# Kernel optimization log

Measured on AMD Instinct MI355X. Metric: run time of the kernel, lower is better.

## Reference

```python
import jax, jax.numpy as jnp
import numpy as np

N, E = 50000, 800000
IN_DIM, HID, H, L = 256, 128, 4, 2
HD = HID // H
EPS = 1e-5


def _bn(x, g, b):
    # training-mode BatchNorm1d: biased variance over batch dim, eps=1e-5
    m = x.mean(0)
    v = jnp.var(x, axis=0)
    return g * (x - m) * jax.lax.rsqrt(v + EPS) + b


def _seg_softmax(scores, dst, n):
    # scores: [E, H]; softmax over edges sharing the same dst node
    m = jax.ops.segment_max(scores, dst, num_segments=n)  # [N, H]
    e = jnp.exp(scores - m[dst])
    s = jax.ops.segment_sum(e, dst, num_segments=n)
    return e / s[dst]


def _attn_layer(h, src, dst, wq, bq, wk, bk, wv, bv, wo, bo):
    n = h.shape[0]
    scale = 1.0 / np.sqrt(HD)
    Q = (h @ wq + bq).reshape(n, H, HD)
    K = (h @ wk + bk).reshape(n, H, HD)
    V = (h @ wv + bv).reshape(n, H, HD)
    # per-edge scores: Q of src dotted with K of dst
    scores = jnp.einsum('ehd,ehd->eh', Q[src], K[dst]) * scale  # [E, H]
    attn = _seg_softmax(scores, dst, n)                         # [E, H]
    # weighted scatter-sum of V gathered at dst (faithful to source)
    out = jax.ops.segment_sum(attn[:, :, None] * V[dst], dst, num_segments=n)
    out = out.reshape(n, HID) @ wo + bo
    return jax.nn.relu(out)


def setup_inputs() -> dict:
    key = jax.random.key(0)
    ks = jax.random.split(key, 20)
    s = 0.05  # weight scale to keep activations tame
    inp = {
        'x': jax.random.normal(ks[0], (N, IN_DIM), jnp.float32),
        'edge_index': jax.random.randint(ks[1], (2, E), 0, N),
        'W_enc1': jax.random.normal(ks[2], (IN_DIM, HID), jnp.float32) * s,
        'b_enc1': jax.random.normal(ks[3], (HID,), jnp.float32) * s,
        'g1': jnp.ones((HID,), jnp.float32),
        'beta1': jnp.zeros((HID,), jnp.float32),
        'W_enc2': jax.random.normal(ks[4], (HID, HID), jnp.float32) * s,
        'b_enc2': jax.random.normal(ks[5], (HID,), jnp.float32) * s,
        'g2': jnp.ones((HID,), jnp.float32),
        'beta2': jnp.zeros((HID,), jnp.float32),
        'Wq': jax.random.normal(ks[6], (L, HID, HID), jnp.float32) * s,
        'bq': jax.random.normal(ks[7], (L, HID), jnp.float32) * s,
        'Wk': jax.random.normal(ks[8], (L, HID, HID), jnp.float32) * s,
        'bk': jax.random.normal(ks[9], (L, HID), jnp.float32) * s,
        'Wv': jax.random.normal(ks[10], (L, HID, HID), jnp.float32) * s,
        'bv': jax.random.normal(ks[11], (L, HID), jnp.float32) * s,
        'Wo': jax.random.normal(ks[12], (L, HID, HID), jnp.float32) * s,
        'bo': jax.random.normal(ks[13], (L, HID), jnp.float32) * s,
    }
    return inp


def reference(x, edge_index, W_enc1, b_enc1, g1, beta1, W_enc2, b_enc2, g2, beta2,
              Wq, bq, Wk, bk, Wv, bv, Wo, bo):
    src, dst = edge_index[0], edge_index[1]
    # encoder: Linear -> BN -> ReLU -> (dropout=id) -> Linear -> BN -> ReLU
    h = jax.nn.relu(_bn(x @ W_enc1 + b_enc1, g1, beta1))
    h = jax.nn.relu(_bn(h @ W_enc2 + b_enc2, g2, beta2))
    for i in range(L):
        h = _attn_layer(h, src, dst, Wq[i], bq[i], Wk[i], bk[i],
                        Wv[i], bv[i], Wo[i], bo[i])
    return h
```

## Files before the change

### kernel.cpp

```cpp
#include <hip/hip_runtime.h>

#define NN 50000
#define NE 800000
#define NB 1563
#define TOTF 114688

typedef unsigned short u16;
typedef unsigned int u32;
typedef __attribute__((ext_vector_type(8))) short s8v;
typedef __attribute__((ext_vector_type(4))) float f4v;

__device__ __forceinline__ void split2(float f, u16& h, u16& lo) {
    u32 u = __float_as_uint(f);
    h = (u16)(u >> 16);
    float r = f - __uint_as_float(u & 0xFFFF0000u);
    lo = (u16)(__float_as_uint(r) >> 16);
}

__global__ void scatter_prep_k(const int* __restrict__ dst, float* __restrict__ mask,
                               const float* __restrict__ W1, const float* __restrict__ W2,
                               const float* __restrict__ Wv, const float* __restrict__ Wo,
                               u16* __restrict__ fh, u16* __restrict__ fl) {
    int i = blockIdx.x * 256 + threadIdx.x;
    if (i < NE) mask[dst[i]] = 1.0f;
    if (i < TOTF) {
        const float* W;
        int local;
        if (i < 32768) { W = W1; local = i; }
        else {
            int t = i - 32768;
            int m = t >> 14;
            local = t & 16383;
            if (m == 0) W = W2;
            else if (m == 1) W = Wv;
            else if (m == 2) W = Wo;
            else if (m == 3) W = Wv + 16384;
            else W = Wo + 16384;
        }
        int j = local & 7, l = (local >> 3) & 63, nt = (local >> 9) & 7, kc = local >> 12;
        int k = kc * 32 + ((l >> 4) << 3) + j;
        int n = nt * 16 + (l & 15);
        u16 h, lo;
        split2(W[k * 128 + n], h, lo);
        fh[i] = h;
        fl[i] = lo;
    }
}

__global__ __launch_bounds__(64)
void redstats_k(const float* __restrict__ pst, float* __restrict__ st) {
    int c = blockIdx.x;
    float s = 0.f;
    for (int b = threadIdx.x; b < NB; b += 64) s += pst[(size_t)c * NB + b];
    s += __shfl_xor(s, 1);  s += __shfl_xor(s, 2);  s += __shfl_xor(s, 4);
    s += __shfl_xor(s, 8);  s += __shfl_xor(s, 16); s += __shfl_xor(s, 32);
    if (threadIdx.x == 0) st[c] = s;
}

template<int KC, int FOLD, int STATS>
__global__ __launch_bounds__(256, 8)
void mgemm_k(const float* __restrict__ A,
             const u16* __restrict__ fh, const u16* __restrict__ fl,
             const float* __restrict__ bias,
             const float* __restrict__ fst,
             const float* __restrict__ fg, const float* __restrict__ fbe,
             float* __restrict__ pst,
             float* __restrict__ C) {
    constexpr int KP = KC / 4;
    __shared__ __align__(16) u16 Ah[32][136];
    __shared__ __align__(16) u16 Al[32][136];
    __shared__ float scl[128], shf[128];
    const int tid = threadIdx.x;
    const int l = tid & 63, w = tid >> 6;
    const int q = l >> 4, cc = l & 15;
    const int sl = w >> 1, hf = w & 1;
    const int row0 = blockIdx.x * 32;

    if (FOLD && tid < 128) {
        float mean = fst[tid] * (1.0f / NN);
        float var = fst[128 + tid] * (1.0f / NN) - mean * mean;
        float rstd = rsqrtf(var + 1e-5f);
        float ga = fg[tid] * rstd;
        scl[tid] = ga;
        shf[tid] = fbe[tid] - mean * ga;
    }

    f4v zf = {0.f, 0.f, 0.f, 0.f};
    f4v acc[4];
#pragma unroll
    for (int t = 0; t < 4; ++t) acc[t] = zf;

    for (int p = 0; p < KP; ++p) {
        if (p > 0 || FOLD) __syncthreads();
#pragma unroll
        for (int it = 0; it < 4; ++it) {
            int lin = tid + 256 * it;
            int r = lin >> 5;
            int c4 = (lin & 31) * 4;
            int gr = row0 + r; if (gr > NN - 1) gr = NN - 1;
            float4 f = *(const float4*)(A + (size_t)gr * (KC * 32) + p * 128 + c4);
            float v[4] = {f.x, f.y, f.z, f.w};
            if (FOLD) {
#pragma unroll
                for (int m = 0; m < 4; ++m) {
                    float t = v[m] * scl[c4 + m] + shf[c4 + m];
                    v[m] = t > 0.f ? t : 0.f;
                }
            }
            ushort4 uh, ul;
            split2(v[0], uh.x, ul.x); split2(v[1], uh.y, ul.y);
            split2(v[2], uh.z, ul.z); split2(v[3], uh.w, ul.w);
            *(ushort4*)&Ah[r][c4] = uh;
            *(ushort4*)&Al[r][c4] = ul;
        }
        __syncthreads();
#pragma unroll
        for (int kc = 0; kc < 4; ++kc) {
            int kcg = p * 4 + kc;
            s8v ah = *(const s8v*)&Ah[16 * sl + cc][kc * 32 + q * 8];
            s8v al = *(const s8v*)&Al[16 * sl + cc][kc * 32 + q * 8];
#pragma unroll
            for (int t = 0; t < 4; ++t) {
                const int fo = kcg * 4096 + (4 * hf + t) * 512 + l * 8;
                s8v bh = *(const s8v*)(fh + fo);
                s8v bl = *(const s8v*)(fl + fo);
                acc[t] = __builtin_amdgcn_mfma_f32_16x16x32_bf16(ah, bh, acc[t], 0, 0, 0);
                acc[t] = __builtin_amdgcn_mfma_f32_16x16x32_bf16(ah, bl, acc[t], 0, 0, 0);
                acc[t] = __builtin_amdgcn_mfma_f32_16x16x32_bf16(al, bh, acc[t], 0, 0, 0);
            }
        }
    }

    float ps[4], pq[4];
#pragma unroll
    for (int t = 0; t < 4; ++t) { ps[t] = 0.f; pq[t] = 0.f; }
#pragma unroll
    for (int t = 0; t < 4; ++t) {
        int col = (4 * hf + t) * 16 + cc;
        float bb = bias[col];
#pragma unroll
        for (int r = 0; r < 4; ++r) {
            int gr = row0 + 16 * sl + q * 4 + r;
            float val = acc[t][r] + bb;
            if (gr < NN) {
                C[(size_t)gr * 128 + col] = val;
                if (STATS) { ps[t] += val; pq[t] += val * val; }
            }
        }
    }
    if (STATS) {
        __syncthreads();
        float* wredS = (float*)&Ah[0][0];
        float* wredQ = wredS + 256;
#pragma unroll
        for (int t = 0; t < 4; ++t) {
            ps[t] += __shfl_xor(ps[t], 16); ps[t] += __shfl_xor(ps[t], 32);
            pq[t] += __shfl_xor(pq[t], 16); pq[t] += __shfl_xor(pq[t], 32);
        }
        if (l < 16) {
#pragma unroll
            for (int t = 0; t < 4; ++t) {
                int col = (4 * hf + t) * 16 + l;
                wredS[sl * 128 + col] = ps[t];
                wredQ[sl * 128 + col] = pq[t];
            }
        }
        __syncthreads();
        int c = tid & 127;
        const float* src = (tid < 128) ? wredS : wredQ;
        pst[(size_t)tid * NB + blockIdx.x] = src[c] + src[128 + c];
    }
}

__global__ __launch_bounds__(256, 8)
void mmega_k(const float* __restrict__ X,
             const u16* __restrict__ fh, const u16* __restrict__ fl,
             const float* __restrict__ bv, const float* __restrict__ bo,
             const float* __restrict__ fst,
             const float* __restrict__ fg, const float* __restrict__ fbe,
             const float* __restrict__ mask, float* __restrict__ out) {
    __shared__ __align__(16) u16 Ah[32][136];
    __shared__ __align__(16) u16 Al[32][136];
    __shared__ float scl[128], shf[128];
    const int tid = threadIdx.x;
    const int l = tid & 63, w = tid >> 6;
    const int q = l >> 4, cc = l & 15;
    const int sl = w >> 1, hf = w & 1;
    const int row0 = blockIdx.x * 32;

    if (tid < 128) {
        float mean = fst[tid] * (1.0f / NN);
        float var = fst[128 + tid] * (1.0f / NN) - mean * mean;
        float rstd = rsqrtf(var + 1e-5f);
        float ga = fg[tid] * rstd;
        scl[tid] = ga;
        shf[tid] = fbe[tid] - mean * ga;
    }
    __syncthreads();

    float rm[4];
#pragma unroll
    for (int r = 0; r < 4; ++r) {
        int gr = row0 + 16 * sl + q * 4 + r;
        rm[r] = (gr < NN) ? mask[gr] : 0.f;
    }

#pragma unroll
    for (int it = 0; it < 4; ++it) {
        int lin = tid + 256 * it;
        int r = lin >> 5;
        int c4 = (lin & 31) * 4;
        int gr = row0 + r; if (gr > NN - 1) gr = NN - 1;
        float4 f = *(const float4*)(X + (size_t)gr * 128 + c4);
        float v[4] = {f.x, f.y, f.z, f.w};
        ushort4 uh, ul;
#pragma unroll
        for (int m = 0; m < 4; ++m) {
            float t = v[m] * scl[c4 + m] + shf[c4 + m];
            v[m] = t > 0.f ? t : 0.f;
        }
        split2(v[0], uh.x, ul.x); split2(v[1], uh.y, ul.y);
        split2(v[2], uh.z, ul.z); split2(v[3], uh.w, ul.w);
        *(ushort4*)&Ah[r][c4] = uh;
        *(ushort4*)&Al[r][c4] = ul;
    }
    __syncthreads();

    f4v zf = {0.f, 0.f, 0.f, 0.f};
    for (int s = 0; s < 4; ++s) {
        const u16* WH = fh + s * 16384;
        const u16* WL = fl + s * 16384;
        const float* bp = (s == 0) ? bv : (s == 1) ? bo : (s == 2) ? (bv + 128) : (bo + 128);

        f4v acc[4];
#pragma unroll
        for (int t = 0; t < 4; ++t) acc[t] = zf;
#pragma unroll
        for (int kc = 0; kc < 4; ++kc) {
            s8v ah = *(const s8v*)&Ah[16 * sl + cc][kc * 32 + q * 8];
            s8v al = *(const s8v*)&Al[16 * sl + cc][kc * 32 + q * 8];
#pragma unroll
            for (int t = 0; t < 4; ++t) {
                const int fo = kc * 4096 + (4 * hf + t) * 512 + l * 8;
                s8v bh = *(const s8v*)(WH + fo);
                s8v bl = *(const s8v*)(WL + fo);
                acc[t] = __builtin_amdgcn_mfma_f32_16x16x32_bf16(ah, bh, acc[t], 0, 0, 0);
                acc[t] = __builtin_amdgcn_mfma_f32_16x16x32_bf16(ah, bl, acc[t], 0, 0, 0);
                acc[t] = __builtin_amdgcn_mfma_f32_16x16x32_bf16(al, bh, acc[t], 0, 0, 0);
            }
        }

        if (s == 3) {
#pragma unroll
            for (int t = 0; t < 4; ++t) {
                int col = (4 * hf + t) * 16 + cc;
                float bb = bp[col];
#pragma unroll
                for (int r = 0; r < 4; ++r) {
                    int gr = row0 + 16 * sl + q * 4 + r;
                    if (gr < NN)
                        out[(size_t)gr * 128 + col] = fmaxf(acc[t][r] + bb, 0.f);
                }
            }
        } else {
            __syncthreads();
#pragma unroll
            for (int t = 0; t < 4; ++t) {
                int col = (4 * hf + t) * 16 + cc;
                float bb = bp[col];
#pragma unroll
                for (int r = 0; r < 4; ++r) {
                    int rl = 16 * sl + q * 4 + r;
                    float val = acc[t][r] + bb;
                    val = (s == 1) ? fmaxf(val, 0.f) : val * rm[r];
                    u16 h, lo; split2(val, h, lo);
                    Ah[rl][col] = h;
                    Al[rl][col] = lo;
                }
            }
            __syncthreads();
        }
    }
}

extern "C" void kernel_launch(void* const* d_in, const int* in_sizes, int n_in,
                              void* d_out, int out_size, void* d_ws, size_t ws_size,
                              hipStream_t stream) {
    const float* x   = (const float*)d_in[0];
    const int*   ei  = (const int*)d_in[1];
    const float* W1  = (const float*)d_in[2];
    const float* b1  = (const float*)d_in[3];
    const float* g1  = (const float*)d_in[4];
    const float* be1 = (const float*)d_in[5];
    const float* W2  = (const float*)d_in[6];
    const float* b2  = (const float*)d_in[7];
    const float* g2  = (const float*)d_in[8];
    const float* be2 = (const float*)d_in[9];
    const float* Wv  = (const float*)d_in[14];
    const float* bv  = (const float*)d_in[15];
    const float* Wo  = (const float*)d_in[16];
    const float* bo  = (const float*)d_in[17];

    float* out = (float*)d_out;

    char* ws = (char*)d_ws;
    float* buf  = (float*)(ws);
    float* mask = (float*)(ws + 25600000);
    float* st1  = (float*)(ws + 25800704);
    float* st2  = st1 + 256;
    u16*   fH   = (u16*)(ws + 25804800);
    u16*   fL   = fH + TOTF;
    float* pst  = (float*)(ws + 26263552);

    hipMemsetAsync(mask, 0, NN * sizeof(float), stream);
    scatter_prep_k<<<dim3((NE + 255) / 256), dim3(256), 0, stream>>>(
        ei + NE, mask, W1, W2, Wv, Wo, fH, fL);

    dim3 gg(NB), bb(256);
    mgemm_k<8, 0, 1><<<gg, bb, 0, stream>>>(x, fH, fL, b1,
                                            nullptr, nullptr, nullptr, pst, buf);
    redstats_k<<<dim3(256), dim3(64), 0, stream>>>(pst, st1);
    mgemm_k<4, 1, 1><<<gg, bb, 0, stream>>>(buf, fH + 32768, fL + 32768, b2,
                                            st1, g1, be1, pst, out);
    redstats_k<<<dim3(256), dim3(64), 0, stream>>>(pst, st2);
    mmega_k<<<gg, bb, 0, stream>>>(out, fH + 49152, fL + 49152, bv, bo,
                                   st2, g2, be2, mask, out);
}
```

Before: 226.3 us.

## Fuse BN stat reduction into GEMM tail via atomic tickets; prefetch next A chunk

```diff
diff --git a/kernel.cpp b/kernel.cpp
--- a/kernel.cpp
+++ b/kernel.cpp
@@ -4,6 +4,7 @@
 #define NE 800000
 #define NB 1563
 #define TOTF 114688
+#define TAILB 256
 
 typedef unsigned short u16;
 typedef unsigned int u32;
@@ -20,8 +21,10 @@
 __global__ void scatter_prep_k(const int* __restrict__ dst, float* __restrict__ mask,
                                const float* __restrict__ W1, const float* __restrict__ W2,
                                const float* __restrict__ Wv, const float* __restrict__ Wo,
-                               u16* __restrict__ fh, u16* __restrict__ fl) {
+                               u16* __restrict__ fh, u16* __restrict__ fl,
+                               u32* __restrict__ tickets) {
     int i = blockIdx.x * 256 + threadIdx.x;
+    if (i < 2) tickets[i] = 0;
     if (i < NE) mask[dst[i]] = 1.0f;
     if (i < TOTF) {
         const float* W;
@@ -47,16 +50,6 @@
     }
 }
 
-__global__ __launch_bounds__(64)
-void redstats_k(const float* __restrict__ pst, float* __restrict__ st) {
-    int c = blockIdx.x;
-    float s = 0.f;
-    for (int b = threadIdx.x; b < NB; b += 64) s += pst[(size_t)c * NB + b];
-    s += __shfl_xor(s, 1);  s += __shfl_xor(s, 2);  s += __shfl_xor(s, 4);
-    s += __shfl_xor(s, 8);  s += __shfl_xor(s, 16); s += __shfl_xor(s, 32);
-    if (threadIdx.x == 0) st[c] = s;
-}
-
 template<int KC, int FOLD, int STATS>
 __global__ __launch_bounds__(256, 8)
 void mgemm_k(const float* __restrict__ A,
@@ -65,11 +58,14 @@
              const float* __restrict__ fst,
              const float* __restrict__ fg, const float* __restrict__ fbe,
              float* __restrict__ pst,
+             u32* __restrict__ tick,
+             float* __restrict__ stout,
              float* __restrict__ C) {
     constexpr int KP = KC / 4;
     __shared__ __align__(16) u16 Ah[32][136];
     __shared__ __align__(16) u16 Al[32][136];
     __shared__ float scl[128], shf[128];
+    __shared__ u32 tkt;
     const int tid = threadIdx.x;
     const int l = tid & 63, w = tid >> 6;
     const int q = l >> 4, cc = l & 15;
@@ -90,6 +86,16 @@
 #pragma unroll
     for (int t = 0; t < 4; ++t) acc[t] = zf;
 
+    float4 pref[4];
+#pragma unroll
+    for (int it = 0; it < 4; ++it) {
+        int lin = tid + 256 * it;
+        int r = lin >> 5;
+        int c4 = (lin & 31) * 4;
+        int gr = row0 + r; if (gr > NN - 1) gr = NN - 1;
+        pref[it] = *(const float4*)(A + (size_t)gr * (KC * 32) + c4);
+    }
+
     for (int p = 0; p < KP; ++p) {
         if (p > 0 || FOLD) __syncthreads();
 #pragma unroll
@@ -97,9 +103,7 @@
             int lin = tid + 256 * it;
             int r = lin >> 5;
             int c4 = (lin & 31) * 4;
-            int gr = row0 + r; if (gr > NN - 1) gr = NN - 1;
-            float4 f = *(const float4*)(A + (size_t)gr * (KC * 32) + p * 128 + c4);
-            float v[4] = {f.x, f.y, f.z, f.w};
+            float v[4] = {pref[it].x, pref[it].y, pref[it].z, pref[it].w};
             if (FOLD) {
 #pragma unroll
                 for (int m = 0; m < 4; ++m) {
@@ -114,6 +118,16 @@
             *(ushort4*)&Al[r][c4] = ul;
         }
         __syncthreads();
+        if (p + 1 < KP) {
+#pragma unroll
+            for (int it = 0; it < 4; ++it) {
+                int lin = tid + 256 * it;
+                int r = lin >> 5;
+                int c4 = (lin & 31) * 4;
+                int gr = row0 + r; if (gr > NN - 1) gr = NN - 1;
+                pref[it] = *(const float4*)(A + (size_t)gr * (KC * 32) + (p + 1) * 128 + c4);
+            }
+        }
 #pragma unroll
         for (int kc = 0; kc < 4; ++kc) {
             int kcg = p * 4 + kc;
@@ -166,9 +180,37 @@
             }
         }
         __syncthreads();
-        int c = tid & 127;
-        const float* src = (tid < 128) ? wredS : wredQ;
-        pst[(size_t)tid * NB + blockIdx.x] = src[c] + src[128 + c];
+        {
+            int c = tid & 127;
+            const float* src = (tid < 128) ? wredS : wredQ;
+            __hip_atomic_store(&pst[(size_t)blockIdx.x * 256 + tid],
+                               src[c] + src[128 + c],
+                               __ATOMIC_RELAXED, __HIP_MEMORY_SCOPE_AGENT);
+        }
+        __syncthreads();
+        if (tid == 0)
+            tkt = __hip_atomic_fetch_add(tick, 1u, __ATOMIC_ACQ_REL,
+                                         __HIP_MEMORY_SCOPE_AGENT);
+        __syncthreads();
+        u32 t = tkt;
+        if (t >= (u32)(NB - TAILB) && t < (u32)NB) {
+            int c = (int)(t - (u32)(NB - TAILB));
+            if (tid == 0) {
+                while (__hip_atomic_load(tick, __ATOMIC_ACQUIRE,
+                                         __HIP_MEMORY_SCOPE_AGENT) < (u32)NB)
+                    __builtin_amdgcn_s_sleep(2);
+            }
+            __syncthreads();
+            if (tid < 64) {
+                float s = 0.f;
+                for (int b = tid; b < NB; b += 64)
+                    s += __hip_atomic_load(&pst[(size_t)b * 256 + c],
+                                           __ATOMIC_RELAXED, __HIP_MEMORY_SCOPE_AGENT);
+                s += __shfl_xor(s, 1);  s += __shfl_xor(s, 2);  s += __shfl_xor(s, 4);
+                s += __shfl_xor(s, 8);  s += __shfl_xor(s, 16); s += __shfl_xor(s, 32);
+                if (tid == 0) stout[c] = s;
+            }
+        }
     }
 }
 
@@ -308,21 +350,22 @@
     float* mask = (float*)(ws + 25600000);
     float* st1  = (float*)(ws + 25800704);
     float* st2  = st1 + 256;
+    u32*   tks  = (u32*)(ws + 25802752);
     u16*   fH   = (u16*)(ws + 25804800);
     u16*   fL   = fH + TOTF;
     float* pst  = (float*)(ws + 26263552);
 
     hipMemsetAsync(mask, 0, NN * sizeof(float), stream);
     scatter_prep_k<<<dim3((NE + 255) / 256), dim3(256), 0, stream>>>(
-        ei + NE, mask, W1, W2, Wv, Wo, fH, fL);
+        ei + NE, mask, W1, W2, Wv, Wo, fH, fL, tks);
 
     dim3 gg(NB), bb(256);
     mgemm_k<8, 0, 1><<<gg, bb, 0, stream>>>(x, fH, fL, b1,
-                                            nullptr, nullptr, nullptr, pst, buf);
-    redstats_k<<<dim3(256), dim3(64), 0, stream>>>(pst, st1);
+                                            nullptr, nullptr, nullptr,
+                                            pst, tks, st1, buf);
     mgemm_k<4, 1, 1><<<gg, bb, 0, stream>>>(buf, fH + 32768, fL + 32768, b2,
-                                            st1, g1, be1, pst, out);
-    redstats_k<<<dim3(256), dim3(64), 0, stream>>>(pst, st2);
+                                            st1, g1, be1,
+                                            pst, tks + 1, st2, out);
     mmega_k<<<gg, bb, 0, stream>>>(out, fH + 49152, fL + 49152, bv, bo,
                                    st2, g2, be2, mask, out);
 }
```

Result: slower. 409.5 us (+81.0%).

## Fold mask scatter into first GEMM, prefetch A tiles, halve mmega block

Applied to the files above, without the earlier changes.

```diff
diff --git a/kernel.cpp b/kernel.cpp
--- a/kernel.cpp
+++ b/kernel.cpp
@@ -3,6 +3,7 @@
 #define NN 50000
 #define NE 800000
 #define NB 1563
+#define NBM 3125
 #define TOTF 114688
 
 typedef unsigned short u16;
@@ -17,12 +18,12 @@
     lo = (u16)(__float_as_uint(r) >> 16);
 }
 
-__global__ void scatter_prep_k(const int* __restrict__ dst, float* __restrict__ mask,
-                               const float* __restrict__ W1, const float* __restrict__ W2,
-                               const float* __restrict__ Wv, const float* __restrict__ Wo,
-                               u16* __restrict__ fh, u16* __restrict__ fl) {
+__global__ void prep_k(float* __restrict__ mask,
+                       const float* __restrict__ W1, const float* __restrict__ W2,
+                       const float* __restrict__ Wv, const float* __restrict__ Wo,
+                       u16* __restrict__ fh, u16* __restrict__ fl) {
     int i = blockIdx.x * 256 + threadIdx.x;
-    if (i < NE) mask[dst[i]] = 1.0f;
+    if (i < NN) mask[i] = 0.f;
     if (i < TOTF) {
         const float* W;
         int local;
@@ -57,13 +58,15 @@
     if (threadIdx.x == 0) st[c] = s;
 }
 
-template<int KC, int FOLD, int STATS>
+template<int KC, int FOLD, int STATS, int SCAT>
 __global__ __launch_bounds__(256, 8)
 void mgemm_k(const float* __restrict__ A,
              const u16* __restrict__ fh, const u16* __restrict__ fl,
              const float* __restrict__ bias,
              const float* __restrict__ fst,
              const float* __restrict__ fg, const float* __restrict__ fbe,
+             const int* __restrict__ dstv,
+             float* __restrict__ maskw,
              float* __restrict__ pst,
              float* __restrict__ C) {
     constexpr int KP = KC / 4;
@@ -76,6 +79,15 @@
     const int sl = w >> 1, hf = w & 1;
     const int row0 = blockIdx.x * 32;
 
+    if (SCAT) {
+        int e2 = (blockIdx.x * 256 + tid) * 2;
+        if (e2 + 1 < NE) {
+            int2 dd = *(const int2*)(dstv + e2);
+            maskw[dd.x] = 1.0f;
+            maskw[dd.y] = 1.0f;
+        }
+    }
+
     if (FOLD && tid < 128) {
         float mean = fst[tid] * (1.0f / NN);
         float var = fst[128 + tid] * (1.0f / NN) - mean * mean;
@@ -90,6 +102,16 @@
 #pragma unroll
     for (int t = 0; t < 4; ++t) acc[t] = zf;
 
+    float4 pref[4];
+#pragma unroll
+    for (int it = 0; it < 4; ++it) {
+        int lin = tid + 256 * it;
+        int r = lin >> 5;
+        int c4 = (lin & 31) * 4;
+        int gr = row0 + r; if (gr > NN - 1) gr = NN - 1;
+        pref[it] = *(const float4*)(A + (size_t)gr * (KC * 32) + c4);
+    }
+
     for (int p = 0; p < KP; ++p) {
         if (p > 0 || FOLD) __syncthreads();
 #pragma unroll
@@ -97,9 +119,7 @@
             int lin = tid + 256 * it;
             int r = lin >> 5;
             int c4 = (lin & 31) * 4;
-            int gr = row0 + r; if (gr > NN - 1) gr = NN - 1;
-            float4 f = *(const float4*)(A + (size_t)gr * (KC * 32) + p * 128 + c4);
-            float v[4] = {f.x, f.y, f.z, f.w};
+            float v[4] = {pref[it].x, pref[it].y, pref[it].z, pref[it].w};
             if (FOLD) {
 #pragma unroll
                 for (int m = 0; m < 4; ++m) {
@@ -114,6 +134,16 @@
             *(ushort4*)&Al[r][c4] = ul;
         }
         __syncthreads();
+        if (p + 1 < KP) {
+#pragma unroll
+            for (int it = 0; it < 4; ++it) {
+                int lin = tid + 256 * it;
+                int r = lin >> 5;
+                int c4 = (lin & 31) * 4;
+                int gr = row0 + r; if (gr > NN - 1) gr = NN - 1;
+                pref[it] = *(const float4*)(A + (size_t)gr * (KC * 32) + (p + 1) * 128 + c4);
+            }
+        }
 #pragma unroll
         for (int kc = 0; kc < 4; ++kc) {
             int kcg = p * 4 + kc;
@@ -172,21 +202,21 @@
     }
 }
 
-__global__ __launch_bounds__(256, 8)
+__global__ __launch_bounds__(128, 8)
 void mmega_k(const float* __restrict__ X,
              const u16* __restrict__ fh, const u16* __restrict__ fl,
              const float* __restrict__ bv, const float* __restrict__ bo,
              const float* __restrict__ fst,
              const float* __restrict__ fg, const float* __restrict__ fbe,
              const float* __restrict__ mask, float* __restrict__ out) {
-    __shared__ __align__(16) u16 Ah[32][136];
-    __shared__ __align__(16) u16 Al[32][136];
+    __shared__ __align__(16) u16 Ah[16][136];
+    __shared__ __align__(16) u16 Al[16][136];
     __shared__ float scl[128], shf[128];
     const int tid = threadIdx.x;
     const int l = tid & 63, w = tid >> 6;
     const int q = l >> 4, cc = l & 15;
-    const int sl = w >> 1, hf = w & 1;
-    const int row0 = blockIdx.x * 32;
+    const int hf = w;
+    const int row0 = blockIdx.x * 16;
 
     if (tid < 128) {
         float mean = fst[tid] * (1.0f / NN);
@@ -201,13 +231,13 @@
     float rm[4];
 #pragma unroll
     for (int r = 0; r < 4; ++r) {
-        int gr = row0 + 16 * sl + q * 4 + r;
+        int gr = row0 + q * 4 + r;
         rm[r] = (gr < NN) ? mask[gr] : 0.f;
     }
 
 #pragma unroll
     for (int it = 0; it < 4; ++it) {
-        int lin = tid + 256 * it;
+        int lin = tid + 128 * it;
         int r = lin >> 5;
         int c4 = (lin & 31) * 4;
         int gr = row0 + r; if (gr > NN - 1) gr = NN - 1;
@@ -237,8 +267,8 @@
         for (int t = 0; t < 4; ++t) acc[t] = zf;
 #pragma unroll
         for (int kc = 0; kc < 4; ++kc) {
-            s8v ah = *(const s8v*)&Ah[16 * sl + cc][kc * 32 + q * 8];
-            s8v al = *(const s8v*)&Al[16 * sl + cc][kc * 32 + q * 8];
+            s8v ah = *(const s8v*)&Ah[cc][kc * 32 + q * 8];
+            s8v al = *(const s8v*)&Al[cc][kc * 32 + q * 8];
 #pragma unroll
             for (int t = 0; t < 4; ++t) {
                 const int fo = kc * 4096 + (4 * hf + t) * 512 + l * 8;
@@ -257,7 +287,7 @@
                 float bb = bp[col];
 #pragma unroll
                 for (int r = 0; r < 4; ++r) {
-                    int gr = row0 + 16 * sl + q * 4 + r;
+                    int gr = row0 + q * 4 + r;
                     if (gr < NN)
                         out[(size_t)gr * 128 + col] = fmaxf(acc[t][r] + bb, 0.f);
                 }
@@ -270,7 +300,7 @@
                 float bb = bp[col];
 #pragma unroll
                 for (int r = 0; r < 4; ++r) {
-                    int rl = 16 * sl + q * 4 + r;
+                    int rl = q * 4 + r;
                     float val = acc[t][r] + bb;
                     val = (s == 1) ? fmaxf(val, 0.f) : val * rm[r];
                     u16 h, lo; split2(val, h, lo);
@@ -312,17 +342,18 @@
     u16*   fL   = fH + TOTF;
     float* pst  = (float*)(ws + 26263552);
 
-    hipMemsetAsync(mask, 0, NN * sizeof(float), stream);
-    scatter_prep_k<<<dim3((NE + 255) / 256), dim3(256), 0, stream>>>(
-        ei + NE, mask, W1, W2, Wv, Wo, fH, fL);
+    prep_k<<<dim3((TOTF + 255) / 256), dim3(256), 0, stream>>>(
+        mask, W1, W2, Wv, Wo, fH, fL);
 
     dim3 gg(NB), bb(256);
-    mgemm_k<8, 0, 1><<<gg, bb, 0, stream>>>(x, fH, fL, b1,
-                                            nullptr, nullptr, nullptr, pst, buf);
+    mgemm_k<8, 0, 1, 1><<<gg, bb, 0, stream>>>(x, fH, fL, b1,
+                                               nullptr, nullptr, nullptr,
+                                               ei + NE, mask, pst, buf);
     redstats_k<<<dim3(256), dim3(64), 0, stream>>>(pst, st1);
-    mgemm_k<4, 1, 1><<<gg, bb, 0, stream>>>(buf, fH + 32768, fL + 32768, b2,
-                                            st1, g1, be1, pst, out);
+    mgemm_k<4, 1, 1, 0><<<gg, bb, 0, stream>>>(buf, fH + 32768, fL + 32768, b2,
+                                               st1, g1, be1,
+                                               nullptr, nullptr, pst, out);
     redstats_k<<<dim3(256), dim3(64), 0, stream>>>(pst, st2);
-    mmega_k<<<gg, bb, 0, stream>>>(out, fH + 49152, fL + 49152, bv, bo,
-                                   st2, g2, be2, mask, out);
-}
+    mmega_k<<<dim3(NBM), dim3(128), 0, stream>>>(out, fH + 49152, fL + 49152, bv, bo,
+                                                 st2, g2, be2, mask, out);
+}
```

Result: faster. 221.3 us (-2.2%).
